# Kernel optimization log

Hardware: AMD Instinct MI355X
Metric: run time of the kernel (lower is better)

## Reference

```python
import jax, jax.numpy as jnp
import numpy as np

B, IN, CTRL, M, V, OUT = 2048, 64, 512, 1024, 64, 64


def setup_inputs() -> dict:
    key = jax.random.key(0)
    ks = jax.random.split(key, 20)
    s = 0.05  # small param scale for numerical stability

    def rn(k, shape, scale):
        return jax.random.normal(k, shape, dtype=jnp.float32) * scale

    return {
        # forward args
        "x": rn(ks[0], (B, IN), 1.0),
        "h_prev": rn(ks[1], (B, CTRL), 0.1),
        "c_prev": rn(ks[2], (B, CTRL), 0.1),
        "read_weights_prev": jax.nn.softmax(rn(ks[3], (B, M), 1.0), axis=1),
        # parameters
        "memory": rn(ks[4], (M, V), 1.0),
        "W_ih": rn(ks[5], (4 * CTRL, IN + V), s),
        "b_ih": rn(ks[6], (4 * CTRL,), s),
        "W_hh": rn(ks[7], (4 * CTRL, CTRL), s),
        "b_hh": rn(ks[8], (4 * CTRL,), s),
        "W_read": rn(ks[9], (M, CTRL), s),
        "b_read": rn(ks[10], (M,), s),
        "W_write": rn(ks[11], (M, CTRL), s),
        "b_write": rn(ks[12], (M,), s),
        "W_erase": rn(ks[13], (V, CTRL), s),
        "b_erase": rn(ks[14], (V,), s),
        "W_add": rn(ks[15], (V, CTRL), s),
        "b_add": rn(ks[16], (V,), s),
        "W_out": rn(ks[17], (OUT, CTRL + V), s),
        "b_out": rn(ks[18], (OUT,), s),
    }


def reference(x, h_prev, c_prev, read_weights_prev, memory,
              W_ih, b_ih, W_hh, b_hh,
              W_read, b_read, W_write, b_write,
              W_erase, b_erase, W_add, b_add,
              W_out, b_out):
    # read with previous weights on pre-write memory: [B,M] @ [M,V] -> [B,V]
    read_prev = read_weights_prev @ memory
    inp = jnp.concatenate([x, read_prev], axis=1)  # [B, IN+V]

    # LSTMCell (PyTorch gate order: i, f, g, o)
    gates = inp @ W_ih.T + b_ih + h_prev @ W_hh.T + b_hh  # [B, 4*CTRL]
    i, f, g, o = jnp.split(gates, 4, axis=1)
    i = jax.nn.sigmoid(i)
    f = jax.nn.sigmoid(f)
    g = jnp.tanh(g)
    o = jax.nn.sigmoid(o)
    c = f * c_prev + i * g
    h = o * jnp.tanh(c)

    # addressing + erase/add vectors
    read_w = jax.nn.softmax(h @ W_read.T + b_read, axis=1)    # [B,M]
    write_w = jax.nn.softmax(h @ W_write.T + b_write, axis=1)  # [B,M]
    erase = jax.nn.sigmoid(h @ W_erase.T + b_erase)            # [B,V]
    add = jnp.tanh(h @ W_add.T + b_add)                        # [B,V]

    # outer-product erase/add memory update: [B,M,V]
    w = write_w[:, :, None]
    mem_new = memory[None, :, :] * (1.0 - w * erase[:, None, :]) + w * add[:, None, :]

    # read with new weights on post-write memory
    read_new = jnp.einsum('bm,bmv->bv', read_w, mem_new)

    out = jnp.concatenate([h, read_new], axis=1) @ W_out.T + b_out  # [B,OUT]
    return out
```

## Files before the change

### kernel.cpp

```cpp
#include <hip/hip_runtime.h>
#include <hip/hip_bf16.h>


typedef unsigned short u16;
typedef __attribute__((ext_vector_type(8))) short bf16x8;
typedef __attribute__((ext_vector_type(4))) float f32x4;

#define MFMA_BF16(a, b, c) __builtin_amdgcn_mfma_f32_16x16x32_bf16((a), (b), (c), 0, 0, 0)
#define LDW 136

__device__ __forceinline__ u16 f2bf(float f) {
    union { float f; unsigned int u; } a; a.f = f;
    return (u16)((a.u + 0x7FFFu + ((a.u >> 16) & 1u)) >> 16);
}

__device__ __forceinline__ void pack_store4(float a0, float a1, float a2, float a3, u16* d) {
    union { __hip_bfloat162 h[2]; uint2 u; } cv;
    cv.h[0] = __float22bfloat162_rn(make_float2(a0, a1));
    cv.h[1] = __float22bfloat162_rn(make_float2(a2, a3));
    *(uint2*)d = cv.u;
}

__device__ __forceinline__ void cvt4(const float* __restrict__ s, u16* __restrict__ d) {
    float4 v = *(const float4*)s;
    pack_store4(v.x, v.y, v.z, v.w, d);
}

__device__ __forceinline__ uint4 cvt8u(const float* __restrict__ s) {
    float4 v0 = *(const float4*)(s);
    float4 v1 = *(const float4*)(s + 4);
    union { __hip_bfloat162 h[4]; uint4 u; } r;
    r.h[0] = __float22bfloat162_rn(make_float2(v0.x, v0.y));
    r.h[1] = __float22bfloat162_rn(make_float2(v0.z, v0.w));
    r.h[2] = __float22bfloat162_rn(make_float2(v1.x, v1.y));
    r.h[3] = __float22bfloat162_rn(make_float2(v1.z, v1.w));
    return r.u;
}

__device__ __forceinline__ uint4 cvt8u_sum4(const float* __restrict__ p, int off) {
    float4 a0 = *(const float4*)(p + off);
    float4 a1 = *(const float4*)(p + 131072 + off);
    float4 a2 = *(const float4*)(p + 262144 + off);
    float4 a3 = *(const float4*)(p + 393216 + off);
    float4 b0 = *(const float4*)(p + off + 4);
    float4 b1 = *(const float4*)(p + 131072 + off + 4);
    float4 b2 = *(const float4*)(p + 262144 + off + 4);
    float4 b3 = *(const float4*)(p + 393216 + off + 4);
    float4 s0{a0.x + a1.x + a2.x + a3.x, a0.y + a1.y + a2.y + a3.y,
              a0.z + a1.z + a2.z + a3.z, a0.w + a1.w + a2.w + a3.w};
    float4 s1{b0.x + b1.x + b2.x + b3.x, b0.y + b1.y + b2.y + b3.y,
              b0.z + b1.z + b2.z + b3.z, b0.w + b1.w + b2.w + b3.w};
    union { __hip_bfloat162 h[4]; uint4 u; } r;
    r.h[0] = __float22bfloat162_rn(make_float2(s0.x, s0.y));
    r.h[1] = __float22bfloat162_rn(make_float2(s0.z, s0.w));
    r.h[2] = __float22bfloat162_rn(make_float2(s1.x, s1.y));
    r.h[3] = __float22bfloat162_rn(make_float2(s1.z, s1.w));
    return r.u;
}

__device__ __forceinline__ float4 bf4_to_f4(uint2 u) {
    union { uint2 u; __hip_bfloat162 h[2]; } c; c.u = u;
    float2 a = __bfloat1622float2(c.h[0]);
    float2 b = __bfloat1622float2(c.h[1]);
    return float4{a.x, a.y, b.x, b.y};
}

__device__ __forceinline__ float sigf(float x) { return 1.f / (1.f + __expf(-x)); }
__device__ __forceinline__ float fast_tanh(float x) { return 1.f - 2.f / (__expf(2.f * x) + 1.f); }

__device__ __forceinline__ float wave_max(float v) {
#pragma unroll
    for (int o = 32; o > 0; o >>= 1) v = fmaxf(v, __shfl_xor(v, o, 64));
    return v;
}
__device__ __forceinline__ float wave_sum(float v) {
#pragma unroll
    for (int o = 32; o > 0; o >>= 1) v += __shfl_xor(v, o, 64);
    return v;
}

__global__ __launch_bounds__(256) void k_pre(
    const float* __restrict__ x, const float* __restrict__ h_prev, const float* __restrict__ rwp,
    const float* __restrict__ memory, const float* __restrict__ W_ih, const float* __restrict__ W_hh,
    const float* __restrict__ W_read, const float* __restrict__ W_write, const float* __restrict__ W_erase,
    const float* __restrict__ W_add, const float* __restrict__ W_out,
    u16* inp_h, u16* wcat, u16* Wcat2, u16* Wo_rn, u16* memt, float* rp)
{
    __shared__ u16 As[64 * LDW];
    __shared__ u16 Bs[64 * LDW];
    const int tid = threadIdx.x;

    if (blockIdx.x < 128) {
        const int mb = blockIdx.x & 31, ks = blockIdx.x >> 5;
        const int w = tid >> 6, lane = tid & 63;
        const int lrow = lane & 15, lq = lane >> 4;
        const int m0 = mb * 64, k0 = ks * 256;
        const int m_loc = tid >> 1, v0 = (tid & 1) * 32;
        f32x4 acc[4] = {};
        for (int kt = 0; kt < 2; ++kt) {
#pragma unroll
            for (int i = 0; i < 4; ++i) {
                int idx = i * 256 + tid, r = idx >> 4, c = (idx & 15) * 8;
                *(uint4*)(&As[r * LDW + c]) = cvt8u(rwp + (m0 + r) * 1024 + k0 + kt * 128 + c);
            }
#pragma unroll
            for (int j = 0; j < 8; ++j) {
                float4 q = *(const float4*)(memory + (k0 + kt * 128 + m_loc) * 64 + v0 + 4 * j);
                Bs[(v0 + 4 * j + 0) * LDW + m_loc] = f2bf(q.x);
                Bs[(v0 + 4 * j + 1) * LDW + m_loc] = f2bf(q.y);
                Bs[(v0 + 4 * j + 2) * LDW + m_loc] = f2bf(q.z);
                Bs[(v0 + 4 * j + 3) * LDW + m_loc] = f2bf(q.w);
            }
            __syncthreads();
#pragma unroll
            for (int kk = 0; kk < 128; kk += 32) {
                bf16x8 a  = *(const bf16x8*)(&As[(16 * w + lrow) * LDW + kk + 8 * lq]);
                bf16x8 b0 = *(const bf16x8*)(&Bs[(lrow) * LDW + kk + 8 * lq]);
                bf16x8 b1 = *(const bf16x8*)(&Bs[(16 + lrow) * LDW + kk + 8 * lq]);
                bf16x8 b2 = *(const bf16x8*)(&Bs[(32 + lrow) * LDW + kk + 8 * lq]);
                bf16x8 b3 = *(const bf16x8*)(&Bs[(48 + lrow) * LDW + kk + 8 * lq]);
                acc[0] = MFMA_BF16(a, b0, acc[0]);
                acc[1] = MFMA_BF16(a, b1, acc[1]);
                acc[2] = MFMA_BF16(a, b2, acc[2]);
                acc[3] = MFMA_BF16(a, b3, acc[3]);
            }
            __syncthreads();
        }
        float* rps = rp + ks * 131072;
#pragma unroll
        for (int nj = 0; nj < 4; ++nj)
#pragma unroll
            for (int r = 0; r < 4; ++r) {
                int row = m0 + 16 * w + 4 * lq + r, col = 16 * nj + lrow;
                rps[row * 64 + col] = acc[nj][r];
            }
        return;
    }

    int t = (blockIdx.x - 128) * 256 + tid;
    if (t < 32768) { int r = t >> 4, c = (t & 15) * 4; cvt4(x + r * 64 + c, inp_h + r * 576 + c); return; }
    t -= 32768;
    if (t < 262144) { int r = t >> 7, c = (t & 127) * 4; cvt4(h_prev + r * 512 + c, inp_h + r * 576 + 64 + c); return; }
    t -= 262144;
    if (t < 65536) {
        int r = t >> 5, c = (t & 31) * 4;
        int g = r >> 9, j = r & 511;
        int rn = (j >> 4) * 64 + (g << 4) + (j & 15);
        int cd = (c < 64) ? c + 64 : c - 64;
        cvt4(W_ih + r * 128 + c, wcat + rn * 640 + cd); return;
    }
    t -= 65536;
    if (t < 262144) {
        int r = t >> 7, c = (t & 127) * 4;
        int g = r >> 9, j = r & 511;
        int rn = (j >> 4) * 64 + (g << 4) + (j & 15);
        cvt4(W_hh + r * 512 + c, wcat + rn * 640 + 128 + c); return;
    }
    t -= 262144;
    if (t < 131072) { cvt4(W_read + t * 4, Wcat2 + t * 4); return; }
    t -= 131072;
    if (t < 131072) { cvt4(W_write + t * 4, Wcat2 + 524288 + t * 4); return; }
    t -= 131072;
    if (t < 8192) { cvt4(W_erase + t * 4, Wcat2 + 1048576 + t * 4); return; }
    t -= 8192;
    if (t < 8192) { cvt4(W_add + t * 4, Wcat2 + 1081344 + t * 4); return; }
    t -= 8192;
    if (t < 9216) {
        int r = t / 144, c = (t % 144) * 4;
        if (c < 512) cvt4(W_out + r * 576 + c, Wcat2 + (2176 + r) * 512 + c);
        else         cvt4(W_out + r * 576 + c, Wo_rn + r * 64 + (c - 512));
        return;
    }
    t -= 9216;
    if (t < 16384) {
        int v = t >> 8, m = (t & 255) * 4;
        pack_store4(memory[m * 64 + v], memory[(m + 1) * 64 + v],
                    memory[(m + 2) * 64 + v], memory[(m + 3) * 64 + v], memt + v * 1024 + m);
    }
}

__global__ __launch_bounds__(256) void k_gates(const u16* __restrict__ inp_h, const float* __restrict__ rp,
                                               const u16* __restrict__ wcat,
                                               const float* __restrict__ b_ih, const float* __restrict__ b_hh,
                                               const float* __restrict__ c_prev, u16* __restrict__ hrn)
{
    __shared__ u16 As[128 * LDW];
    __shared__ u16 Bs[64 * LDW];
    const int tid = threadIdx.x, w = tid >> 6, lane = tid & 63;
    const int lrow = lane & 15, lq = lane >> 4;
    const int m0 = blockIdx.x * 128, bn = blockIdx.y;
    const u16* Bbase = wcat + bn * 64 * 640;
    f32x4 acc[2][4] = {};
    for (int kt = 0; kt < 5; ++kt) {
#pragma unroll
        for (int i = 0; i < 8; ++i) {
            int idx = i * 256 + tid, r = idx >> 4, c = (idx & 15) * 8;
            int ak = kt * 128 + c;
            uint4 v;
            if (ak < 64) v = cvt8u_sum4(rp, (m0 + r) * 64 + ak);
            else         v = *(const uint4*)(inp_h + (m0 + r) * 576 + (ak - 64));
            *(uint4*)(&As[r * LDW + c]) = v;
        }
#pragma unroll
        for (int i = 0; i < 4; ++i) {
            int idx = i * 256 + tid, r = idx >> 4, c = (idx & 15) * 8;
            *(uint4*)(&Bs[r * LDW + c]) = *(const uint4*)(Bbase + r * 640 + kt * 128 + c);
        }
        __syncthreads();
#pragma unroll
        for (int kk = 0; kk < 128; kk += 32) {
            bf16x8 a0 = *(const bf16x8*)(&As[(32 * w + lrow) * LDW + kk + 8 * lq]);
            bf16x8 a1 = *(const bf16x8*)(&As[(32 * w + 16 + lrow) * LDW + kk + 8 * lq]);
            bf16x8 b0 = *(const bf16x8*)(&Bs[(lrow) * LDW + kk + 8 * lq]);
            bf16x8 b1 = *(const bf16x8*)(&Bs[(16 + lrow) * LDW + kk + 8 * lq]);
            bf16x8 b2 = *(const bf16x8*)(&Bs[(32 + lrow) * LDW + kk + 8 * lq]);
            bf16x8 b3 = *(const bf16x8*)(&Bs[(48 + lrow) * LDW + kk + 8 * lq]);
            acc[0][0] = MFMA_BF16(a0, b0, acc[0][0]);
            acc[0][1] = MFMA_BF16(a0, b1, acc[0][1]);
            acc[0][2] = MFMA_BF16(a0, b2, acc[0][2]);
            acc[0][3] = MFMA_BF16(a0, b3, acc[0][3]);
            acc[1][0] = MFMA_BF16(a1, b0, acc[1][0]);
            acc[1][1] = MFMA_BF16(a1, b1, acc[1][1]);
            acc[1][2] = MFMA_BF16(a1, b2, acc[1][2]);
            acc[1][3] = MFMA_BF16(a1, b3, acc[1][3]);
        }
        __syncthreads();
    }
    const int j = bn * 16 + lrow;
    const float bI = b_ih[j] + b_hh[j];
    const float bF = b_ih[512 + j] + b_hh[512 + j];
    const float bG = b_ih[1024 + j] + b_hh[1024 + j];
    const float bO = b_ih[1536 + j] + b_hh[1536 + j];
#pragma unroll
    for (int mi = 0; mi < 2; ++mi)
#pragma unroll
        for (int r = 0; r < 4; ++r) {
            int row = m0 + 32 * w + 16 * mi + 4 * lq + r;
            float ig = sigf(acc[mi][0][r] + bI);
            float fg = sigf(acc[mi][1][r] + bF);
            float gg = fast_tanh(acc[mi][2][r] + bG);
            float og = sigf(acc[mi][3][r] + bO);
            float c = fg * c_prev[row * 512 + j] + ig * gg;
            hrn[row * 512 + j] = f2bf(og * fast_tanh(c));
        }
}

__global__ __launch_bounds__(256) void k_heads(const u16* __restrict__ hrn, const u16* __restrict__ Wcat2,
                                               const float* __restrict__ b_read, const float* __restrict__ b_write,
                                               const float* __restrict__ b_erase, const float* __restrict__ b_add,
                                               const float* __restrict__ b_out,
                                               u16* __restrict__ pre_r, u16* __restrict__ pre_w,
                                               float* __restrict__ erase, float* __restrict__ add,
                                               float* __restrict__ out)
{
    __shared__ u16 As[128 * LDW];
    __shared__ u16 Bs[64 * LDW];
    const int tid = threadIdx.x, w = tid >> 6, lane = tid & 63;
    const int lrow = lane & 15, lq = lane >> 4;
    const int m0 = blockIdx.x * 128, bn = blockIdx.y;
    const u16* Bbase = Wcat2 + bn * 64 * 512;
    f32x4 acc[2][4] = {};
    for (int kt = 0; kt < 4; ++kt) {
#pragma unroll
        for (int i = 0; i < 8; ++i) {
            int idx = i * 256 + tid, r = idx >> 4, c = (idx & 15) * 8;
            *(uint4*)(&As[r * LDW + c]) = *(const uint4*)(hrn + (m0 + r) * 512 + kt * 128 + c);
        }
#pragma unroll
        for (int i = 0; i < 4; ++i) {
            int idx = i * 256 + tid, r = idx >> 4, c = (idx & 15) * 8;
            *(uint4*)(&Bs[r * LDW + c]) = *(const uint4*)(Bbase + r * 512 + kt * 128 + c);
        }
        __syncthreads();
#pragma unroll
        for (int kk = 0; kk < 128; kk += 32) {
            bf16x8 a0 = *(const bf16x8*)(&As[(32 * w + lrow) * LDW + kk + 8 * lq]);
            bf16x8 a1 = *(const bf16x8*)(&As[(32 * w + 16 + lrow) * LDW + kk + 8 * lq]);
            bf16x8 b0 = *(const bf16x8*)(&Bs[(lrow) * LDW + kk + 8 * lq]);
            bf16x8 b1 = *(const bf16x8*)(&Bs[(16 + lrow) * LDW + kk + 8 * lq]);
            bf16x8 b2 = *(const bf16x8*)(&Bs[(32 + lrow) * LDW + kk + 8 * lq]);
            bf16x8 b3 = *(const bf16x8*)(&Bs[(48 + lrow) * LDW + kk + 8 * lq]);
            acc[0][0] = MFMA_BF16(a0, b0, acc[0][0]);
            acc[0][1] = MFMA_BF16(a0, b1, acc[0][1]);
            acc[0][2] = MFMA_BF16(a0, b2, acc[0][2]);
            acc[0][3] = MFMA_BF16(a0, b3, acc[0][3]);
            acc[1][0] = MFMA_BF16(a1, b0, acc[1][0]);
            acc[1][1] = MFMA_BF16(a1, b1, acc[1][1]);
            acc[1][2] = MFMA_BF16(a1, b2, acc[1][2]);
            acc[1][3] = MFMA_BF16(a1, b3, acc[1][3]);
        }
        __syncthreads();
    }
#pragma unroll
    for (int mi = 0; mi < 2; ++mi)
#pragma unroll
        for (int nj = 0; nj < 4; ++nj)
#pragma unroll
            for (int r = 0; r < 4; ++r) {
                int row = m0 + 32 * w + 16 * mi + 4 * lq + r;
                int col = bn * 64 + 16 * nj + lrow;
                float v = acc[mi][nj][r];
                if (bn < 16)       pre_r[row * 1024 + col] = f2bf(v + b_read[col]);
                else if (bn < 32)  pre_w[row * 1024 + (col - 1024)] = f2bf(v + b_write[col - 1024]);
                else if (bn == 32) erase[row * 64 + (col - 2048)] = sigf(v + b_erase[col - 2048]);
                else if (bn == 33) add[row * 64 + (col - 2112)] = fast_tanh(v + b_add[col - 2112]);
                else               out[row * 64 + (col - 2176)] = v + b_out[col - 2176];
            }
}

__global__ __launch_bounds__(256) void k_softmax(const u16* __restrict__ pr, const u16* __restrict__ pw,
                                                 u16* __restrict__ rw_bf, u16* __restrict__ rw2_bf,
                                                 float* __restrict__ s)
{
    int b = blockIdx.x, tid = threadIdx.x, w = tid >> 6, lane = tid & 63;
    float4 vr = bf4_to_f4(*(const uint2*)(pr + b * 1024 + tid * 4));
    float4 vw = bf4_to_f4(*(const uint2*)(pw + b * 1024 + tid * 4));
    float mr = fmaxf(fmaxf(vr.x, vr.y), fmaxf(vr.z, vr.w));
    float mw = fmaxf(fmaxf(vw.x, vw.y), fmaxf(vw.z, vw.w));
    mr = wave_max(mr); mw = wave_max(mw);
    __shared__ float red[4][4];
    if (lane == 0) { red[0][w] = mr; red[1][w] = mw; }
    __syncthreads();
    mr = fmaxf(fmaxf(red[0][0], red[0][1]), fmaxf(red[0][2], red[0][3]));
    mw = fmaxf(fmaxf(red[1][0], red[1][1]), fmaxf(red[1][2], red[1][3]));
    float er[4] = {__expf(vr.x - mr), __expf(vr.y - mr), __expf(vr.z - mr), __expf(vr.w - mr)};
    float ew[4] = {__expf(vw.x - mw), __expf(vw.y - mw), __expf(vw.z - mw), __expf(vw.w - mw)};
    float sr = er[0] + er[1] + er[2] + er[3];
    float sw = ew[0] + ew[1] + ew[2] + ew[3];
    sr = wave_sum(sr); sw = wave_sum(sw);
    __syncthreads();
    if (lane == 0) { red[2][w] = sr; red[3][w] = sw; }
    __syncthreads();
    sr = red[2][0] + red[2][1] + red[2][2] + red[2][3];
    sw = red[3][0] + red[3][1] + red[3][2] + red[3][3];
    float isr = 1.f / sr, isw = 1.f / sw, ss = 0.f;
    float a[4], r2[4];
#pragma unroll
    for (int i = 0; i < 4; ++i) {
        a[i] = er[i] * isr;
        r2[i] = a[i] * (ew[i] * isw);
        ss += r2[i];
    }
    pack_store4(a[0], a[1], a[2], a[3], rw_bf + b * 1024 + tid * 4);
    pack_store4(r2[0], r2[1], r2[2], r2[3], rw2_bf + b * 1024 + tid * 4);
    ss = wave_sum(ss);
    __syncthreads();
    if (lane == 0) red[0][w] = ss;
    __syncthreads();
    if (tid == 0) s[b] = red[0][0] + red[0][1] + red[0][2] + red[0][3];
}

__global__ __launch_bounds__(256) void k_rnout(const u16* __restrict__ rw, const u16* __restrict__ rw2,
                                               const u16* __restrict__ memt, const u16* __restrict__ Wo_rn,
                                               const float* __restrict__ erase, const float* __restrict__ add,
                                               const float* __restrict__ s, float* __restrict__ out)
{
    __shared__ u16 As1[32 * LDW];
    __shared__ u16 As2[32 * LDW];
    __shared__ u16 Bs[64 * LDW];
    __shared__ u16 Ps[32 * 72];
    const int tid = threadIdx.x, w = tid >> 6, lane = tid & 63;
    const int lrow = lane & 15, lq = lane >> 4;
    const int m0 = blockIdx.x * 32, k0 = blockIdx.y * 256;
    const int mt = w & 1, nb = (w >> 1) * 2;

    f32x4 a1[2] = {}, a2[2] = {};
    for (int kt = 0; kt < 2; ++kt) {
#pragma unroll
        for (int i = 0; i < 2; ++i) {
            int idx = i * 256 + tid, r = idx >> 4, c = (idx & 15) * 8;
            *(uint4*)(&As1[r * LDW + c]) = *(const uint4*)(rw + (m0 + r) * 1024 + k0 + kt * 128 + c);
            *(uint4*)(&As2[r * LDW + c]) = *(const uint4*)(rw2 + (m0 + r) * 1024 + k0 + kt * 128 + c);
        }
#pragma unroll
        for (int i = 0; i < 4; ++i) {
            int idx = i * 256 + tid, r = idx >> 4, c = (idx & 15) * 8;
            *(uint4*)(&Bs[r * LDW + c]) = *(const uint4*)(memt + r * 1024 + k0 + kt * 128 + c);
        }
        __syncthreads();
#pragma unroll
        for (int kk = 0; kk < 128; kk += 32) {
            bf16x8 a  = *(const bf16x8*)(&As1[(16 * mt + lrow) * LDW + kk + 8 * lq]);
            bf16x8 c2 = *(const bf16x8*)(&As2[(16 * mt + lrow) * LDW + kk + 8 * lq]);
            bf16x8 b0 = *(const bf16x8*)(&Bs[(16 * nb + lrow) * LDW + kk + 8 * lq]);
            bf16x8 b1 = *(const bf16x8*)(&Bs[(16 * (nb + 1) + lrow) * LDW + kk + 8 * lq]);
            a1[0] = MFMA_BF16(a, b0, a1[0]);
            a1[1] = MFMA_BF16(a, b1, a1[1]);
            a2[0] = MFMA_BF16(c2, b0, a2[0]);
            a2[1] = MFMA_BF16(c2, b1, a2[1]);
        }
        __syncthreads();
    }
#pragma unroll
    for (int i = 0; i < 2; ++i) {
        int idx = i * 256 + tid, r = idx >> 3, c = (idx & 7) * 8;
        *(uint4*)(&Bs[r * LDW + c]) = *(const uint4*)(Wo_rn + r * 64 + c);
    }
#pragma unroll
    for (int j = 0; j < 2; ++j)
#pragma unroll
        for (int r = 0; r < 4; ++r) {
            int row_l = 16 * mt + 4 * lq + r, col = 16 * (nb + j) + lrow;
            int row_g = m0 + row_l;
            float p = a1[j][r] - erase[row_g * 64 + col] * a2[j][r];
            if (blockIdx.y == 0) p += add[row_g * 64 + col] * s[row_g];
            Ps[row_l * 72 + col] = f2bf(p);
        }
    __syncthreads();
    f32x4 o[2] = {};
#pragma unroll
    for (int kk = 0; kk < 64; kk += 32) {
        bf16x8 a  = *(const bf16x8*)(&Ps[(16 * mt + lrow) * 72 + kk + 8 * lq]);
        bf16x8 b0 = *(const bf16x8*)(&Bs[(16 * nb + lrow) * LDW + kk + 8 * lq]);
        bf16x8 b1 = *(const bf16x8*)(&Bs[(16 * (nb + 1) + lrow) * LDW + kk + 8 * lq]);
        o[0] = MFMA_BF16(a, b0, o[0]);
        o[1] = MFMA_BF16(a, b1, o[1]);
    }
#pragma unroll
    for (int j = 0; j < 2; ++j)
#pragma unroll
        for (int r = 0; r < 4; ++r) {
            int row_g = m0 + 16 * mt + 4 * lq + r, col = 16 * (nb + j) + lrow;
            atomicAdd(&out[row_g * 64 + col], o[j][r]);
        }
}

extern "C" void kernel_launch(void* const* d_in, const int* in_sizes, int n_in,
                              void* d_out, int out_size, void* d_ws, size_t ws_size,
                              hipStream_t stream)
{
    const float* x        = (const float*)d_in[0];
    const float* h_prev   = (const float*)d_in[1];
    const float* c_prev   = (const float*)d_in[2];
    const float* rwp      = (const float*)d_in[3];
    const float* memory   = (const float*)d_in[4];
    const float* W_ih     = (const float*)d_in[5];
    const float* b_ih     = (const float*)d_in[6];
    const float* W_hh     = (const float*)d_in[7];
    const float* b_hh     = (const float*)d_in[8];
    const float* W_read   = (const float*)d_in[9];
    const float* b_read   = (const float*)d_in[10];
    const float* W_write  = (const float*)d_in[11];
    const float* b_write  = (const float*)d_in[12];
    const float* W_erase  = (const float*)d_in[13];
    const float* b_erase  = (const float*)d_in[14];
    const float* W_add    = (const float*)d_in[15];
    const float* b_add    = (const float*)d_in[16];
    const float* W_out    = (const float*)d_in[17];
    const float* b_out    = (const float*)d_in[18];
    float* out = (float*)d_out;

    char* wsp = (char*)d_ws;
    u16*   inp_h  = (u16*)(wsp + 0);
    u16*   wcat   = (u16*)(wsp + 2359296);
    u16*   memt   = (u16*)(wsp + 4980736);
    u16*   Wcat2  = (u16*)(wsp + 5111808);
    u16*   Wo_rn  = (u16*)(wsp + 7405568);
    float* rp     = (float*)(wsp + 7413760);
    u16*   hrn    = (u16*)(wsp + 9510912);
    u16*   pre_r  = (u16*)(wsp + 11608064);
    u16*   pre_w  = (u16*)(wsp + 15802368);
    float* erase  = (float*)(wsp + 19996672);
    float* add    = (float*)(wsp + 20520960);
    u16*   rw_bf  = (u16*)(wsp + 21045248);
    u16*   rw2_bf = (u16*)(wsp + 25239552);
    float* s_buf  = (float*)(wsp + 29433856);

    k_pre<<<3748, 256, 0, stream>>>(x, h_prev, rwp, memory, W_ih, W_hh, W_read, W_write,
                                    W_erase, W_add, W_out,
                                    inp_h, wcat, Wcat2, Wo_rn, memt, rp);
    k_gates<<<dim3(16, 32), 256, 0, stream>>>(inp_h, rp, wcat, b_ih, b_hh, c_prev, hrn);
    k_heads<<<dim3(16, 35), 256, 0, stream>>>(hrn, Wcat2, b_read, b_write, b_erase, b_add, b_out,
                                              pre_r, pre_w, erase, add, out);
    k_softmax<<<2048, 256, 0, stream>>>(pre_r, pre_w, rw_bf, rw2_bf, s_buf);
    k_rnout<<<dim3(64, 4), 256, 0, stream>>>(rw_bf, rw2_bf, memt, Wo_rn, erase, add, s_buf, out);
}
```

Baseline: 159.8 us.

## Fuse softmax into the read/output tail kernel, dropping the rw intermediate buffers

Merges the softmax kernel and the read-new/output GEMM kernel into one k_tail kernel. Each block computes the softmaxes for 16 rows in registers and keeps its half of the read and combined weights in shared memory, so the bf16 rw/rw2 buffers no longer round-trip through global memory and one launch is removed. In exchange each block of the two K-halves recomputes the full softmax of its rows (duplicated work), the grid shrinks to 256 blocks, and each thread holds 128 floats in registers, which may limit occupancy.

```diff
diff --git a/kernel.cpp b/kernel.cpp
--- a/kernel.cpp
+++ b/kernel.cpp
@@ -58,26 +58,22 @@
     return r.u;
 }
 
-__device__ __forceinline__ float4 bf4_to_f4(uint2 u) {
-    union { uint2 u; __hip_bfloat162 h[2]; } c; c.u = u;
-    float2 a = __bfloat1622float2(c.h[0]);
-    float2 b = __bfloat1622float2(c.h[1]);
-    return float4{a.x, a.y, b.x, b.y};
+__device__ __forceinline__ void bfu4_to_f8(uint4 u, float* f) {
+    f[0] = __uint_as_float(u.x << 16); f[1] = __uint_as_float(u.x & 0xffff0000u);
+    f[2] = __uint_as_float(u.y << 16); f[3] = __uint_as_float(u.y & 0xffff0000u);
+    f[4] = __uint_as_float(u.z << 16); f[5] = __uint_as_float(u.z & 0xffff0000u);
+    f[6] = __uint_as_float(u.w << 16); f[7] = __uint_as_float(u.w & 0xffff0000u);
+}
+
+__device__ __forceinline__ uint4 pack8(const float* v) {
+    union { __hip_bfloat162 h[4]; uint4 u; } r;
+#pragma unroll
+    for (int j = 0; j < 4; ++j) r.h[j] = __float22bfloat162_rn(make_float2(v[2 * j], v[2 * j + 1]));
+    return r.u;
 }
 
 __device__ __forceinline__ float sigf(float x) { return 1.f / (1.f + __expf(-x)); }
 __device__ __forceinline__ float fast_tanh(float x) { return 1.f - 2.f / (__expf(2.f * x) + 1.f); }
-
-__device__ __forceinline__ float wave_max(float v) {
-#pragma unroll
-    for (int o = 32; o > 0; o >>= 1) v = fmaxf(v, __shfl_xor(v, o, 64));
-    return v;
-}
-__device__ __forceinline__ float wave_sum(float v) {
-#pragma unroll
-    for (int o = 32; o > 0; o >>= 1) v += __shfl_xor(v, o, 64);
-    return v;
-}
 
 __global__ __launch_bounds__(256) void k_pre(
     const float* __restrict__ x, const float* __restrict__ h_prev, const float* __restrict__ rwp,
@@ -308,121 +304,123 @@
             }
 }
 
-__global__ __launch_bounds__(256) void k_softmax(const u16* __restrict__ pr, const u16* __restrict__ pw,
-                                                 u16* __restrict__ rw_bf, u16* __restrict__ rw2_bf,
-                                                 float* __restrict__ s)
+#define SLDW 520
+
+__global__ __launch_bounds__(256) void k_tail(const u16* __restrict__ pre_r, const u16* __restrict__ pre_w,
+                                              const u16* __restrict__ memt, const u16* __restrict__ Wo_rn,
+                                              const float* __restrict__ erase, const float* __restrict__ add,
+                                              float* __restrict__ out)
 {
-    int b = blockIdx.x, tid = threadIdx.x, w = tid >> 6, lane = tid & 63;
-    float4 vr = bf4_to_f4(*(const uint2*)(pr + b * 1024 + tid * 4));
-    float4 vw = bf4_to_f4(*(const uint2*)(pw + b * 1024 + tid * 4));
-    float mr = fmaxf(fmaxf(vr.x, vr.y), fmaxf(vr.z, vr.w));
-    float mw = fmaxf(fmaxf(vw.x, vw.y), fmaxf(vw.z, vw.w));
-    mr = wave_max(mr); mw = wave_max(mw);
-    __shared__ float red[4][4];
-    if (lane == 0) { red[0][w] = mr; red[1][w] = mw; }
-    __syncthreads();
-    mr = fmaxf(fmaxf(red[0][0], red[0][1]), fmaxf(red[0][2], red[0][3]));
-    mw = fmaxf(fmaxf(red[1][0], red[1][1]), fmaxf(red[1][2], red[1][3]));
-    float er[4] = {__expf(vr.x - mr), __expf(vr.y - mr), __expf(vr.z - mr), __expf(vr.w - mr)};
-    float ew[4] = {__expf(vw.x - mw), __expf(vw.y - mw), __expf(vw.z - mw), __expf(vw.w - mw)};
-    float sr = er[0] + er[1] + er[2] + er[3];
-    float sw = ew[0] + ew[1] + ew[2] + ew[3];
-    sr = wave_sum(sr); sw = wave_sum(sw);
-    __syncthreads();
-    if (lane == 0) { red[2][w] = sr; red[3][w] = sw; }
-    __syncthreads();
-    sr = red[2][0] + red[2][1] + red[2][2] + red[2][3];
-    sw = red[3][0] + red[3][1] + red[3][2] + red[3][3];
-    float isr = 1.f / sr, isw = 1.f / sw, ss = 0.f;
-    float a[4], r2[4];
-#pragma unroll
-    for (int i = 0; i < 4; ++i) {
-        a[i] = er[i] * isr;
-        r2[i] = a[i] * (ew[i] * isw);
-        ss += r2[i];
-    }
-    pack_store4(a[0], a[1], a[2], a[3], rw_bf + b * 1024 + tid * 4);
-    pack_store4(r2[0], r2[1], r2[2], r2[3], rw2_bf + b * 1024 + tid * 4);
-    ss = wave_sum(ss);
-    __syncthreads();
-    if (lane == 0) red[0][w] = ss;
-    __syncthreads();
-    if (tid == 0) s[b] = red[0][0] + red[0][1] + red[0][2] + red[0][3];
-}
-
-__global__ __launch_bounds__(256) void k_rnout(const u16* __restrict__ rw, const u16* __restrict__ rw2,
-                                               const u16* __restrict__ memt, const u16* __restrict__ Wo_rn,
-                                               const float* __restrict__ erase, const float* __restrict__ add,
-                                               const float* __restrict__ s, float* __restrict__ out)
-{
-    __shared__ u16 As1[32 * LDW];
-    __shared__ u16 As2[32 * LDW];
-    __shared__ u16 Bs[64 * LDW];
-    __shared__ u16 Ps[32 * 72];
+    __shared__ u16 rwS[16 * SLDW];
+    __shared__ u16 rw2S[16 * SLDW];
+    __shared__ u16 BsP[64 * LDW];
+    __shared__ u16 Ps[16 * 72];
+    __shared__ float s_sh[16];
     const int tid = threadIdx.x, w = tid >> 6, lane = tid & 63;
     const int lrow = lane & 15, lq = lane >> 4;
-    const int m0 = blockIdx.x * 32, k0 = blockIdx.y * 256;
-    const int mt = w & 1, nb = (w >> 1) * 2;
-
-    f32x4 a1[2] = {}, a2[2] = {};
-    for (int kt = 0; kt < 2; ++kt) {
-#pragma unroll
-        for (int i = 0; i < 2; ++i) {
-            int idx = i * 256 + tid, r = idx >> 4, c = (idx & 15) * 8;
-            *(uint4*)(&As1[r * LDW + c]) = *(const uint4*)(rw + (m0 + r) * 1024 + k0 + kt * 128 + c);
-            *(uint4*)(&As2[r * LDW + c]) = *(const uint4*)(rw2 + (m0 + r) * 1024 + k0 + kt * 128 + c);
-        }
+    const int mb = blockIdx.x >> 1, kh = blockIdx.x & 1;
+    const int m0 = mb * 16, k0 = kh * 512;
+
+    {
+        const int row = tid >> 4, c16 = tid & 15;
+        const int row_g = m0 + row;
+        const u16* prp = pre_r + row_g * 1024;
+        const u16* pwp = pre_w + row_g * 1024;
+        float vr[64], vw[64];
+#pragma unroll
+        for (int q = 0; q < 8; ++q) {
+            bfu4_to_f8(*(const uint4*)(prp + q * 128 + c16 * 8), vr + 8 * q);
+            bfu4_to_f8(*(const uint4*)(pwp + q * 128 + c16 * 8), vw + 8 * q);
+        }
+        float mr = vr[0], mw = vw[0];
+#pragma unroll
+        for (int i = 1; i < 64; ++i) { mr = fmaxf(mr, vr[i]); mw = fmaxf(mw, vw[i]); }
+#pragma unroll
+        for (int o = 1; o < 16; o <<= 1) {
+            mr = fmaxf(mr, __shfl_xor(mr, o, 64));
+            mw = fmaxf(mw, __shfl_xor(mw, o, 64));
+        }
+        float sr = 0.f, sw = 0.f;
+#pragma unroll
+        for (int i = 0; i < 64; ++i) {
+            vr[i] = __expf(vr[i] - mr); sr += vr[i];
+            vw[i] = __expf(vw[i] - mw); sw += vw[i];
+        }
+#pragma unroll
+        for (int o = 1; o < 16; o <<= 1) {
+            sr += __shfl_xor(sr, o, 64);
+            sw += __shfl_xor(sw, o, 64);
+        }
+        const float isr = 1.f / sr, isw = 1.f / sw;
+        float ss = 0.f;
+#pragma unroll
+        for (int q = 0; q < 8; ++q) {
+            float a8[8], r8[8];
+#pragma unroll
+            for (int i = 0; i < 8; ++i) {
+                float a = vr[8 * q + i] * isr;
+                float r2 = a * (vw[8 * q + i] * isw);
+                a8[i] = a; r8[i] = r2;
+                ss += r2;
+            }
+            if ((q >> 2) == kh) {
+                int cb = (q - 4 * kh) * 128 + c16 * 8;
+                *(uint4*)(&rwS[row * SLDW + cb])  = pack8(a8);
+                *(uint4*)(&rw2S[row * SLDW + cb]) = pack8(r8);
+            }
+        }
+#pragma unroll
+        for (int o = 1; o < 16; o <<= 1) ss += __shfl_xor(ss, o, 64);
+        if (c16 == 0) s_sh[row] = ss;
+    }
+    __syncthreads();
+
+    f32x4 acc1 = {}, acc2 = {};
+    for (int kt = 0; kt < 4; ++kt) {
 #pragma unroll
         for (int i = 0; i < 4; ++i) {
             int idx = i * 256 + tid, r = idx >> 4, c = (idx & 15) * 8;
-            *(uint4*)(&Bs[r * LDW + c]) = *(const uint4*)(memt + r * 1024 + k0 + kt * 128 + c);
+            *(uint4*)(&BsP[r * LDW + c]) = *(const uint4*)(memt + r * 1024 + k0 + kt * 128 + c);
         }
         __syncthreads();
 #pragma unroll
         for (int kk = 0; kk < 128; kk += 32) {
-            bf16x8 a  = *(const bf16x8*)(&As1[(16 * mt + lrow) * LDW + kk + 8 * lq]);
-            bf16x8 c2 = *(const bf16x8*)(&As2[(16 * mt + lrow) * LDW + kk + 8 * lq]);
-            bf16x8 b0 = *(const bf16x8*)(&Bs[(16 * nb + lrow) * LDW + kk + 8 * lq]);
-            bf16x8 b1 = *(const bf16x8*)(&Bs[(16 * (nb + 1) + lrow) * LDW + kk + 8 * lq]);
-            a1[0] = MFMA_BF16(a, b0, a1[0]);
-            a1[1] = MFMA_BF16(a, b1, a1[1]);
-            a2[0] = MFMA_BF16(c2, b0, a2[0]);
-            a2[1] = MFMA_BF16(c2, b1, a2[1]);
-        }
-        __syncthreads();
+            bf16x8 a1 = *(const bf16x8*)(&rwS[lrow * SLDW + kt * 128 + kk + 8 * lq]);
+            bf16x8 a2 = *(const bf16x8*)(&rw2S[lrow * SLDW + kt * 128 + kk + 8 * lq]);
+            bf16x8 b  = *(const bf16x8*)(&BsP[(16 * w + lrow) * LDW + kk + 8 * lq]);
+            acc1 = MFMA_BF16(a1, b, acc1);
+            acc2 = MFMA_BF16(a2, b, acc2);
+        }
+        __syncthreads();
+    }
+
+#pragma unroll
+    for (int r = 0; r < 4; ++r) {
+        int row_l = 4 * lq + r, col = 16 * w + lrow;
+        int row_g = m0 + row_l;
+        float p = acc1[r] - erase[row_g * 64 + col] * acc2[r];
+        if (kh == 0) p += add[row_g * 64 + col] * s_sh[row_l];
+        Ps[row_l * 72 + col] = f2bf(p);
     }
 #pragma unroll
     for (int i = 0; i < 2; ++i) {
         int idx = i * 256 + tid, r = idx >> 3, c = (idx & 7) * 8;
-        *(uint4*)(&Bs[r * LDW + c]) = *(const uint4*)(Wo_rn + r * 64 + c);
-    }
-#pragma unroll
-    for (int j = 0; j < 2; ++j)
-#pragma unroll
-        for (int r = 0; r < 4; ++r) {
-            int row_l = 16 * mt + 4 * lq + r, col = 16 * (nb + j) + lrow;
-            int row_g = m0 + row_l;
-            float p = a1[j][r] - erase[row_g * 64 + col] * a2[j][r];
-            if (blockIdx.y == 0) p += add[row_g * 64 + col] * s[row_g];
-            Ps[row_l * 72 + col] = f2bf(p);
-        }
+        *(uint4*)(&BsP[r * LDW + c]) = *(const uint4*)(Wo_rn + r * 64 + c);
+    }
     __syncthreads();
-    f32x4 o[2] = {};
+
+    f32x4 acc3 = {};
 #pragma unroll
     for (int kk = 0; kk < 64; kk += 32) {
-        bf16x8 a  = *(const bf16x8*)(&Ps[(16 * mt + lrow) * 72 + kk + 8 * lq]);
-        bf16x8 b0 = *(const bf16x8*)(&Bs[(16 * nb + lrow) * LDW + kk + 8 * lq]);
-        bf16x8 b1 = *(const bf16x8*)(&Bs[(16 * (nb + 1) + lrow) * LDW + kk + 8 * lq]);
-        o[0] = MFMA_BF16(a, b0, o[0]);
-        o[1] = MFMA_BF16(a, b1, o[1]);
-    }
-#pragma unroll
-    for (int j = 0; j < 2; ++j)
-#pragma unroll
-        for (int r = 0; r < 4; ++r) {
-            int row_g = m0 + 16 * mt + 4 * lq + r, col = 16 * (nb + j) + lrow;
-            atomicAdd(&out[row_g * 64 + col], o[j][r]);
-        }
+        bf16x8 a = *(const bf16x8*)(&Ps[lrow * 72 + kk + 8 * lq]);
+        bf16x8 b = *(const bf16x8*)(&BsP[(16 * w + lrow) * LDW + kk + 8 * lq]);
+        acc3 = MFMA_BF16(a, b, acc3);
+    }
+#pragma unroll
+    for (int r = 0; r < 4; ++r) {
+        int row_g = m0 + 4 * lq + r, col = 16 * w + lrow;
+        atomicAdd(&out[row_g * 64 + col], acc3[r]);
+    }
 }
 
 extern "C" void kernel_launch(void* const* d_in, const int* in_sizes, int n_in,
@@ -462,9 +460,6 @@
     u16*   pre_w  = (u16*)(wsp + 15802368);
     float* erase  = (float*)(wsp + 19996672);
     float* add    = (float*)(wsp + 20520960);
-    u16*   rw_bf  = (u16*)(wsp + 21045248);
-    u16*   rw2_bf = (u16*)(wsp + 25239552);
-    float* s_buf  = (float*)(wsp + 29433856);
 
     k_pre<<<3748, 256, 0, stream>>>(x, h_prev, rwp, memory, W_ih, W_hh, W_read, W_write,
                                     W_erase, W_add, W_out,
@@ -472,6 +467,5 @@
     k_gates<<<dim3(16, 32), 256, 0, stream>>>(inp_h, rp, wcat, b_ih, b_hh, c_prev, hrn);
     k_heads<<<dim3(16, 35), 256, 0, stream>>>(hrn, Wcat2, b_read, b_write, b_erase, b_add, b_out,
                                               pre_r, pre_w, erase, add, out);
-    k_softmax<<<2048, 256, 0, stream>>>(pre_r, pre_w, rw_bf, rw2_bf, s_buf);
-    k_rnout<<<dim3(64, 4), 256, 0, stream>>>(rw_bf, rw2_bf, memt, Wo_rn, erase, add, s_buf, out);
-}
+    k_tail<<<256, 256, 0, stream>>>(pre_r, pre_w, memt, Wo_rn, erase, add, out);
+}
```

Result: no change. 159.1 us (-0.5%).
